# Optimization experiments

Hardware: AMD Instinct MI355X
Metric: run time of the kernel (lower is better)

## Reference

```python
import jax, jax.numpy as jnp
import numpy as np

N, M, ND, K = 80000, 150000, 10000, 27  # active voxels, 2D painted points, downscaled voxels, 3x3x3 kernel
C3, C2, CP = 16, 64, 259                # 3D ch (stage 1), 2D conv ch, painted 2D feature ch
CM, CO = C3 + C2, 32 + 64               # mixed ch (80), downscale out ch (96)


def subm_conv(feats, nbr, W):
    """Submanifold sparse conv as gather + per-offset GEMM.
    feats: [N_in, Cin], nbr: [N_out, K] int (-1 = missing), W: [K, Cin, Cout]."""
    out = jnp.zeros((nbr.shape[0], W.shape[-1]), feats.dtype)
    for k in range(W.shape[0]):  # fixed small kernel loop (27)
        idx = nbr[:, k]
        g = jnp.where((idx >= 0)[:, None], feats[jnp.clip(idx, 0)], 0.0)
        out = out + g @ W[k]
    return out


def bn_relu(x, gamma, beta):  # folded eval-mode BN1d + ReLU
    return jax.nn.relu(x * gamma + beta)


def setup_inputs() -> dict:
    key = jax.random.key(0)
    ks = jax.random.split(key, 24)

    def w(k, shape, fan_in):
        return jax.random.normal(k, shape, jnp.float32) * (1.0 / np.sqrt(fan_in))

    inp = {
        'x3d': jax.random.normal(ks[0], (N, C3), jnp.float32),
        'f2d': jax.random.normal(ks[1], (M, CP), jnp.float32),
        'nn_idx': jax.random.randint(ks[2], (N,), -1, M, jnp.int32),     # -1 = no 2D match
        'nbr': jax.random.randint(ks[3], (N, K), -1, N, jnp.int32),      # -1 = missing neighbor
        'nbr_ds': jax.random.randint(ks[4], (ND, K), -1, N, jnp.int32),
        'W3d': w(ks[5], (K, C3, C3), K * C3),
        'g3d': jnp.ones((C3,), jnp.float32), 'b3d': jnp.zeros((C3,), jnp.float32),
        'Wg': w(ks[6], (C3, CP), C3), 'bg': jnp.zeros((CP,), jnp.float32),
        'Wc': w(ks[7], (C3, CP), C3), 'bc': jnp.zeros((CP,), jnp.float32),
        'Wp': w(ks[8], (CP, C2), CP),
        'W2d': w(ks[9], (K, C2, C2), K * C2),
        'g2d': jnp.ones((C2,), jnp.float32), 'b2d': jnp.zeros((C2,), jnp.float32),
        'Wm1': w(ks[10], (K, CM, CM), K * CM),
        'gm1': jnp.ones((CM,), jnp.float32), 'bm1': jnp.zeros((CM,), jnp.float32),
        'Wm2': w(ks[11], (K, CM, CM), K * CM),
        'gm2': jnp.ones((CM,), jnp.float32), 'bm2': jnp.zeros((CM,), jnp.float32),
        'Wa1': w(ks[12], (K, CM, CM), K * CM),
        'ga1': jnp.ones((CM,), jnp.float32), 'ba1': jnp.zeros((CM,), jnp.float32),
        'Wa2': w(ks[13], (K, CM, CM), K * CM),
        'ga2': jnp.ones((CM,), jnp.float32), 'ba2': jnp.zeros((CM,), jnp.float32),
        'Wds': w(ks[14], (K, CM, CO), K * CM),
        'gds': jnp.ones((CO,), jnp.float32), 'bds': jnp.zeros((CO,), jnp.float32),
    }
    return inp


def reference(x3d, f2d, nn_idx, nbr, nbr_ds,
              W3d, g3d, b3d, Wg, bg, Wc, bc, Wp,
              W2d, g2d, b2d,
              Wm1, gm1, bm1, Wm2, gm2, bm2,
              Wa1, ga1, ba1, Wa2, ga2, ba2,
              Wds, gds, bds):
    # irregular gather of painted 2D features to voxel sites (NN index, -1 invalid)
    f2g = jnp.where((nn_idx >= 0)[:, None], f2d[jnp.clip(nn_idx, 0)], 0.0)  # [N, 259]

    # 3D branch: SubMConv3d(C3->C3) + BN + ReLU
    y3d = bn_relu(subm_conv(x3d, nbr, W3d), g3d, b3d)                       # [N, 16]

    # per-stage gate / cross-gate (Linear + ReLU) on 3D features, applied to raw 2D feats
    gate = jax.nn.relu(y3d @ Wg + bg)                                       # [N, 259]
    cross = jax.nn.relu(y3d @ Wc + bc)                                      # [N, 259]

    # gated 2D branch: project gated painted feats to 64, SubMConv3d + BN + ReLU
    p2d = (gate * f2g) @ Wp                                                 # [N, 64]
    x2d = bn_relu(subm_conv(p2d, nbr, W2d), g2d, b2d)                       # [N, 64]
    cross2d = (cross * f2g) @ Wp                                            # [N, 64]

    # cross-modal mix + SparseBasicBlock (residual, two subm convs)
    mix = jnp.concatenate([y3d, x2d + cross2d], axis=-1)                    # [N, 80]
    h = bn_relu(subm_conv(mix, nbr, Wm1), gm1, bm1)
    h = jax.nn.relu(subm_conv(h, nbr, Wm2) * gm2 + bm2 + mix)

    # aggregation SparseBasicBlock
    a = bn_relu(subm_conv(h, nbr, Wa1), ga1, ba1)
    a = jax.nn.relu(subm_conv(a, nbr, Wa2) * ga2 + ba2 + h)

    # strided SparseConv3d downscale (gather from input sites at new out sites)
    out = bn_relu(subm_conv(a, nbr_ds, Wds), gds, bds)                      # [ND, 96]
    return out
```

## Files before the change

kernel.cpp:

```cpp
#include <hip/hip_runtime.h>

#define NPTS 80000
#define MPTS 150000
#define NDPTS 10000
#define KOFF 27
#define C3 16
#define CP 259
#define C2 64
#define CM 80
#define CO 96

typedef __attribute__((ext_vector_type(8))) short short8;
typedef __attribute__((ext_vector_type(4))) float f32x4;

__device__ inline short bf16r(float f) {
  union { float f; unsigned u; } x{f};
  unsigned r = (x.u + 0x7fffu + ((x.u >> 16) & 1u)) >> 16;
  return (short)r;
}

__global__ void wfrag_kernel(const float* __restrict__ W, short* __restrict__ WbfF,
                             int CIN, int COUT_, int KC) {
  const int NT = COUT_ / 16;
  int i = blockIdx.x * 256 + threadIdx.x;
  int total = KOFF * KC * NT * 512;
  if (i >= total) return;
  int j = i & 7, lane = (i >> 3) & 63;
  int rest = i >> 9;
  int t = rest % NT; rest /= NT;
  int q = rest % KC;
  int k = rest / KC;
  int ci = q * 32 + (lane >> 4) * 8 + j;
  int n = t * 16 + (lane & 15);
  float v = (ci < CIN) ? W[((size_t)k * CIN + ci) * COUT_ + n] : 0.f;
  WbfF[i] = bf16r(v);
}

__global__ void wpfrag_kernel(const float* __restrict__ Wp, short* __restrict__ WpF) {
  int i = blockIdx.x * 256 + threadIdx.x;
  if (i >= 9 * 4 * 64 * 8) return;
  int j = i & 7, lane = (i >> 3) & 63, t = (i >> 9) & 3, q = i >> 11;
  int k = q * 32 + (lane >> 4) * 8 + j;
  int n = t * 16 + (lane & 15);
  WpF[i] = (k < CP) ? bf16r(Wp[(size_t)k * C2 + n]) : (short)0;
}

__global__ __launch_bounds__(256) void conv3d_bnrelu_kernel(
    const float* __restrict__ x3d, const int* __restrict__ nbr,
    const float* __restrict__ W3d, const float* __restrict__ g3d,
    const float* __restrict__ b3d, float* __restrict__ y3d,
    float* __restrict__ mix, short* __restrict__ mixbf)
{
  __shared__ float wS[KOFF * C3 * C3];
  __shared__ float fS[16][C3];
  const int tid = threadIdx.x;
  const int base = blockIdx.x * 16;
  for (int e = tid; e < KOFF * C3 * C3; e += 256) wS[e] = W3d[e];
  const int r = tid >> 4, c = tid & 15;
  const int row = base + r;
  float acc = 0.f;
  for (int k = 0; k < KOFF; ++k) {
    int idx = nbr[row * KOFF + k];
    float fv = (idx >= 0) ? x3d[idx * C3 + c] : 0.f;
    __syncthreads();
    fS[r][c] = fv;
    __syncthreads();
    const float* wk = &wS[k * C3 * C3];
    #pragma unroll
    for (int ci = 0; ci < C3; ++ci)
      acc = fmaf(fS[r][ci], wk[ci * C3 + c], acc);
  }
  float v = fmaxf(fmaf(acc, g3d[c], b3d[c]), 0.f);
  y3d[row * C3 + c] = v;
  mix[row * CM + c] = v;
  mixbf[row * CM + c] = bf16r(v);
}

__global__ __launch_bounds__(256) void gate_cross_mfma_kernel(
    const float* __restrict__ y3d, const float* __restrict__ f2d,
    const int* __restrict__ nn_idx,
    const float* __restrict__ Wg, const float* __restrict__ bg,
    const float* __restrict__ Wc, const float* __restrict__ bc,
    const short* __restrict__ WpF,
    short* __restrict__ p2dbf, float* __restrict__ cross2d)
{
  constexpr int RS = 296;
  __shared__ short g1S[32 * RS];
  __shared__ short g2S[32 * RS];
  const int tid = threadIdx.x;
  const int lane = tid & 63;
  const int w = tid >> 6;
  const int lm = lane & 15;
  const int quad = lane >> 4;
  const int base = blockIdx.x * 32;

  for (int e = tid; e < 32 * 32; e += 256) {
    int r = e >> 5, cc = 256 + (e & 31);
    if (cc >= CP) {
      g1S[r * RS + cc] = 0;
      g2S[r * RS + cc] = 0;
    }
  }

  {
    const int c = tid;
    float wg[16], wc[16];
    #pragma unroll
    for (int ci = 0; ci < 16; ++ci) {
      wg[ci] = Wg[ci * CP + c];
      wc[ci] = Wc[ci * CP + c];
    }
    const float bgv = bg[c], bcv = bc[c];
    for (int r = 0; r < 32; ++r) {
      const int row = base + r;
      const int idx = nn_idx[row];
      const float* yr = y3d + (size_t)row * C3;
      float f = (idx >= 0) ? f2d[(size_t)idx * CP + c] : 0.f;
      float a1 = bgv, a2 = bcv;
      #pragma unroll
      for (int ci = 0; ci < 16; ++ci) {
        float yv = yr[ci];
        a1 = fmaf(yv, wg[ci], a1);
        a2 = fmaf(yv, wc[ci], a2);
      }
      g1S[r * RS + c] = bf16r(fmaxf(a1, 0.f) * f);
      g2S[r * RS + c] = bf16r(fmaxf(a2, 0.f) * f);
    }
  }
  if (w == 0 && lane < 3) {
    const int c = 256 + lane;
    float wg[16], wc[16];
    #pragma unroll
    for (int ci = 0; ci < 16; ++ci) {
      wg[ci] = Wg[ci * CP + c];
      wc[ci] = Wc[ci * CP + c];
    }
    const float bgv = bg[c], bcv = bc[c];
    for (int r = 0; r < 32; ++r) {
      const int row = base + r;
      const int idx = nn_idx[row];
      const float* yr = y3d + (size_t)row * C3;
      float f = (idx >= 0) ? f2d[(size_t)idx * CP + c] : 0.f;
      float a1 = bgv, a2 = bcv;
      #pragma unroll
      for (int ci = 0; ci < 16; ++ci) {
        float yv = yr[ci];
        a1 = fmaf(yv, wg[ci], a1);
        a2 = fmaf(yv, wc[ci], a2);
      }
      g1S[r * RS + c] = bf16r(fmaxf(a1, 0.f) * f);
      g2S[r * RS + c] = bf16r(fmaxf(a2, 0.f) * f);
    }
  }
  __syncthreads();

  const int gsel = w & 1;
  const int mt = w >> 1;
  const short* gS = gsel ? g2S : g1S;
  f32x4 acc[4];
  #pragma unroll
  for (int t = 0; t < 4; ++t) {
    f32x4 z = {0.f, 0.f, 0.f, 0.f};
    acc[t] = z;
  }
  #pragma unroll
  for (int q = 0; q < 9; ++q) {
    short8 af = *(const short8*)&gS[(mt * 16 + lm) * RS + q * 32 + quad * 8];
    #pragma unroll
    for (int t = 0; t < 4; ++t) {
      short8 bf = *(const short8*)&WpF[(((q * 4 + t) * 64) + lane) * 8];
      acc[t] = __builtin_amdgcn_mfma_f32_16x16x32_bf16(af, bf, acc[t], 0, 0, 0);
    }
  }
  #pragma unroll
  for (int t = 0; t < 4; ++t) {
    const int c = t * 16 + lm;
    #pragma unroll
    for (int rg = 0; rg < 4; ++rg) {
      const int row = base + mt * 16 + quad * 4 + rg;
      float v = acc[t][rg];
      if (gsel == 0)
        p2dbf[(size_t)row * C2 + c] = bf16r(v);
      else
        cross2d[(size_t)row * C2 + c] = v;
    }
  }
}

template <int CIN, int COUT_, int MODE, int MINW>
__global__ __launch_bounds__(256, MINW) void conv_db_kernel(
    const short* __restrict__ finbf, const int* __restrict__ nbr, int nrows,
    const short* __restrict__ WbfF, const float* __restrict__ gamma,
    const float* __restrict__ beta, const float* __restrict__ resf,
    float* __restrict__ outf, short* __restrict__ outbf)
{
  constexpr int KC = (CIN + 31) / 32;
  constexpr int KC32 = KC * 32;
  constexpr int AS = KC32 + 8;
  constexpr int PCH = KC32 / 8;
  constexpr int DCH = CIN / 8;
  constexpr int NT = COUT_ / 16;
  constexpr int MT = 2;
  constexpr int ROWS = 128;
  constexpr int AR = ROWS * PCH / 256;

  __shared__ short fA[2][ROWS * AS];

  const int tid = threadIdx.x;
  const int lane = tid & 63;
  const int w = tid >> 6;
  const int lm = lane & 15;
  const int quad = lane >> 4;
  const int base = blockIdx.x * ROWS;

  int ar[AR], ac[AR];
  #pragma unroll
  for (int i = 0; i < AR; ++i) {
    int j = tid + i * 256;
    ar[i] = j / PCH;
    ac[i] = j - ar[i] * PCH;
  }

  f32x4 acc[MT][NT];
  #pragma unroll
  for (int i = 0; i < MT; ++i)
    #pragma unroll
    for (int t = 0; t < NT; ++t) {
      f32x4 z = {0.f, 0.f, 0.f, 0.f};
      acc[i][t] = z;
    }

  const short8 zero8 = {0, 0, 0, 0, 0, 0, 0, 0};
  short8 pa[AR];

  #pragma unroll
  for (int i = 0; i < AR; ++i) {
    int row = base + ar[i];
    int ix = (row < nrows) ? nbr[(size_t)row * KOFF] : -1;
    pa[i] = (ix >= 0 && ac[i] < DCH)
        ? *(const short8*)&finbf[(size_t)ix * CIN + ac[i] * 8] : zero8;
  }
  #pragma unroll
  for (int i = 0; i < AR; ++i)
    *(short8*)&fA[0][ar[i] * AS + ac[i] * 8] = pa[i];
  __syncthreads();

  for (int k = 0; k < KOFF; ++k) {
    const int cur = k & 1;
    if (k + 1 < KOFF) {
      #pragma unroll
      for (int i = 0; i < AR; ++i) {
        int row = base + ar[i];
        int ix = (row < nrows) ? nbr[(size_t)row * KOFF + k + 1] : -1;
        pa[i] = (ix >= 0 && ac[i] < DCH)
            ? *(const short8*)&finbf[(size_t)ix * CIN + ac[i] * 8] : zero8;
      }
    }
    #pragma unroll
    for (int q = 0; q < KC; ++q) {
      short8 afr[MT];
      #pragma unroll
      for (int i = 0; i < MT; ++i)
        afr[i] = *(const short8*)&fA[cur][((w * MT + i) * 16 + lm) * AS +
                                          q * 32 + quad * 8];
      #pragma unroll
      for (int t = 0; t < NT; ++t) {
        short8 bfr = *(const short8*)&WbfF[(size_t)(((k * KC + q) * NT + t) * 512) +
                                           lane * 8];
        #pragma unroll
        for (int i = 0; i < MT; ++i)
          acc[i][t] = __builtin_amdgcn_mfma_f32_16x16x32_bf16(afr[i], bfr,
                                                              acc[i][t], 0, 0, 0);
      }
    }
    if (k + 1 < KOFF) {
      #pragma unroll
      for (int i = 0; i < AR; ++i)
        *(short8*)&fA[cur ^ 1][ar[i] * AS + ac[i] * 8] = pa[i];
    }
    __syncthreads();
  }

  #pragma unroll
  for (int i = 0; i < MT; ++i) {
    int rbase = base + (w * MT + i) * 16 + quad * 4;
    #pragma unroll
    for (int t = 0; t < NT; ++t) {
      int c = t * 16 + lm;
      float g = gamma[c], b = beta[c];
      #pragma unroll
      for (int rg = 0; rg < 4; ++rg) {
        int row = rbase + rg;
        if (row >= nrows) continue;
        float v = acc[i][t][rg];
        if (MODE == 0) {
          outf[(size_t)row * COUT_ + c] = fmaxf(fmaf(v, g, b), 0.f);
        } else if (MODE == 1) {
          outbf[(size_t)row * COUT_ + c] = bf16r(fmaxf(fmaf(v, g, b), 0.f));
        } else if (MODE == 2) {
          float o = fmaxf(fmaf(v, g, b), 0.f) + resf[(size_t)row * C2 + c];
          outf[(size_t)row * CM + 16 + c] = o;
          outbf[(size_t)row * CM + 16 + c] = bf16r(o);
        } else if (MODE == 3) {
          float o = fmaxf(fmaf(v, g, b) + resf[(size_t)row * COUT_ + c], 0.f);
          outf[(size_t)row * COUT_ + c] = o;
          outbf[(size_t)row * COUT_ + c] = bf16r(o);
        } else {
          float o = fmaxf(fmaf(v, g, b) + resf[(size_t)row * COUT_ + c], 0.f);
          outbf[(size_t)row * COUT_ + c] = bf16r(o);
        }
      }
    }
  }
}

extern "C" void kernel_launch(void* const* d_in, const int* in_sizes, int n_in,
                              void* d_out, int out_size, void* d_ws, size_t ws_size,
                              hipStream_t stream) {
  const float* x3d  = (const float*)d_in[0];
  const float* f2d  = (const float*)d_in[1];
  const int*   nn   = (const int*)d_in[2];
  const int*   nbr  = (const int*)d_in[3];
  const int*   nbds = (const int*)d_in[4];
  const float* W3d  = (const float*)d_in[5];
  const float* g3d  = (const float*)d_in[6];
  const float* b3d  = (const float*)d_in[7];
  const float* Wg   = (const float*)d_in[8];
  const float* bg   = (const float*)d_in[9];
  const float* Wc   = (const float*)d_in[10];
  const float* bc   = (const float*)d_in[11];
  const float* Wp   = (const float*)d_in[12];
  const float* W2d  = (const float*)d_in[13];
  const float* g2d  = (const float*)d_in[14];
  const float* b2d  = (const float*)d_in[15];
  const float* Wm1  = (const float*)d_in[16];
  const float* gm1  = (const float*)d_in[17];
  const float* bm1  = (const float*)d_in[18];
  const float* Wm2  = (const float*)d_in[19];
  const float* gm2  = (const float*)d_in[20];
  const float* bm2  = (const float*)d_in[21];
  const float* Wa1  = (const float*)d_in[22];
  const float* ga1  = (const float*)d_in[23];
  const float* ba1  = (const float*)d_in[24];
  const float* Wa2  = (const float*)d_in[25];
  const float* ga2  = (const float*)d_in[26];
  const float* ba2  = (const float*)d_in[27];
  const float* Wds  = (const float*)d_in[28];
  const float* gds  = (const float*)d_in[29];
  const float* bds  = (const float*)d_in[30];

  const size_t N = NPTS;
  float* ws = (float*)d_ws;
  float* y3d     = ws;
  short* p2dbf   = (short*)(ws + N * 16);
  float* cross2d = ws + N * 48;
  float* mix     = ws + N * 112;
  short* mixbf   = (short*)(ws + N * 192);
  short* tmp1bf  = (short*)(ws + N * 232);
  float* hbuf    = ws + N * 272;
  short* hbufbf  = (short*)(ws + N * 352);
  short* abufbf  = (short*)ws;
  short* wtail  = (short*)(ws + N * 392);
  short* WbfF2d = wtail;
  short* WbfFm1 = WbfF2d + 110592;
  short* WbfFm2 = WbfFm1 + 207360;
  short* WbfFa1 = WbfFm2 + 207360;
  short* WbfFa2 = WbfFa1 + 207360;
  short* WbfFds = WbfFa2 + 207360;
  short* WpF    = WbfFds + 248832;

  wfrag_kernel<<<(110592 + 255) / 256, 256, 0, stream>>>(W2d, WbfF2d, 64, 64, 2);
  wfrag_kernel<<<(207360 + 255) / 256, 256, 0, stream>>>(Wm1, WbfFm1, 80, 80, 3);
  wfrag_kernel<<<(207360 + 255) / 256, 256, 0, stream>>>(Wm2, WbfFm2, 80, 80, 3);
  wfrag_kernel<<<(207360 + 255) / 256, 256, 0, stream>>>(Wa1, WbfFa1, 80, 80, 3);
  wfrag_kernel<<<(207360 + 255) / 256, 256, 0, stream>>>(Wa2, WbfFa2, 80, 80, 3);
  wfrag_kernel<<<(248832 + 255) / 256, 256, 0, stream>>>(Wds, WbfFds, 80, 96, 3);
  wpfrag_kernel<<<(9 * 4 * 64 * 8 + 255) / 256, 256, 0, stream>>>(Wp, WpF);

  conv3d_bnrelu_kernel<<<NPTS / 16, 256, 0, stream>>>(x3d, nbr, W3d, g3d, b3d,
                                                      y3d, mix, mixbf);
  gate_cross_mfma_kernel<<<NPTS / 32, 256, 0, stream>>>(y3d, f2d, nn, Wg, bg,
                                                        Wc, bc, WpF, p2dbf,
                                                        cross2d);

  const int gridN = (NPTS + 127) / 128;
  conv_db_kernel<64, 64, 2, 4><<<gridN, 256, 0, stream>>>(
      p2dbf, nbr, NPTS, WbfF2d, g2d, b2d, cross2d, mix, mixbf);
  conv_db_kernel<80, 80, 1, 3><<<gridN, 256, 0, stream>>>(
      mixbf, nbr, NPTS, WbfFm1, gm1, bm1, nullptr, nullptr, tmp1bf);
  conv_db_kernel<80, 80, 3, 3><<<gridN, 256, 0, stream>>>(
      tmp1bf, nbr, NPTS, WbfFm2, gm2, bm2, mix, hbuf, hbufbf);
  conv_db_kernel<80, 80, 1, 3><<<gridN, 256, 0, stream>>>(
      hbufbf, nbr, NPTS, WbfFa1, ga1, ba1, nullptr, nullptr, tmp1bf);
  conv_db_kernel<80, 80, 4, 3><<<gridN, 256, 0, stream>>>(
      tmp1bf, nbr, NPTS, WbfFa2, ga2, ba2, hbuf, nullptr, abufbf);

  const int gridND = (NDPTS + 127) / 128;
  conv_db_kernel<80, 96, 0, 3><<<gridND, 256, 0, stream>>>(
      abufbf, nbds, NDPTS, WbfFds, gds, bds, nullptr, (float*)d_out, nullptr);
}
```

Measured before the change: 1.136 ms.

## Replace LDS double-buffered sparse conv with register-direct gather and triple-buffered prefetch

The sparse conv kernel no longer stages gathered neighbor rows through shared memory. Each 64-thread wave loads its MFMA A-fragments straight from global memory into registers, using a three-stage rotation of register buffers and neighbor indices to prefetch offsets ahead of the MFMAs. This removes the LDS writes and reads and the per-offset __syncthreads. In exchange it raises register pressure, and the gathers are narrower and less coalesced. Blocks shrink to one wave covering 32 rows, which gives many more small blocks.

```diff
diff --git a/kernel.cpp b/kernel.cpp
--- a/kernel.cpp
+++ b/kernel.cpp
@@ -187,38 +187,29 @@
   }
 }
 
-template <int CIN, int COUT_, int MODE, int MINW>
-__global__ __launch_bounds__(256, MINW) void conv_db_kernel(
+template <int CIN, int COUT_, int MODE>
+__global__ __launch_bounds__(64, 2) void conv_nolds_kernel(
     const short* __restrict__ finbf, const int* __restrict__ nbr, int nrows,
     const short* __restrict__ WbfF, const float* __restrict__ gamma,
     const float* __restrict__ beta, const float* __restrict__ resf,
     float* __restrict__ outf, short* __restrict__ outbf)
 {
   constexpr int KC = (CIN + 31) / 32;
-  constexpr int KC32 = KC * 32;
-  constexpr int AS = KC32 + 8;
-  constexpr int PCH = KC32 / 8;
   constexpr int DCH = CIN / 8;
   constexpr int NT = COUT_ / 16;
   constexpr int MT = 2;
-  constexpr int ROWS = 128;
-  constexpr int AR = ROWS * PCH / 256;
-
-  __shared__ short fA[2][ROWS * AS];
-
-  const int tid = threadIdx.x;
-  const int lane = tid & 63;
-  const int w = tid >> 6;
+
+  const int lane = threadIdx.x;
   const int lm = lane & 15;
   const int quad = lane >> 4;
-  const int base = blockIdx.x * ROWS;
-
-  int ar[AR], ac[AR];
-  #pragma unroll
-  for (int i = 0; i < AR; ++i) {
-    int j = tid + i * 256;
-    ar[i] = j / PCH;
-    ac[i] = j - ar[i] * PCH;
+  const int base = blockIdx.x * (MT * 16);
+
+  int rrow[MT];
+  bool rok[MT];
+  #pragma unroll
+  for (int i = 0; i < MT; ++i) {
+    rrow[i] = base + i * 16 + lm;
+    rok[i] = rrow[i] < nrows;
   }
 
   f32x4 acc[MT][NT];
@@ -231,59 +222,63 @@
     }
 
   const short8 zero8 = {0, 0, 0, 0, 0, 0, 0, 0};
-  short8 pa[AR];
-
-  #pragma unroll
-  for (int i = 0; i < AR; ++i) {
-    int row = base + ar[i];
-    int ix = (row < nrows) ? nbr[(size_t)row * KOFF] : -1;
-    pa[i] = (ix >= 0 && ac[i] < DCH)
-        ? *(const short8*)&finbf[(size_t)ix * CIN + ac[i] * 8] : zero8;
-  }
-  #pragma unroll
-  for (int i = 0; i < AR; ++i)
-    *(short8*)&fA[0][ar[i] * AS + ac[i] * 8] = pa[i];
-  __syncthreads();
-
-  for (int k = 0; k < KOFF; ++k) {
-    const int cur = k & 1;
-    if (k + 1 < KOFF) {
-      #pragma unroll
-      for (int i = 0; i < AR; ++i) {
-        int row = base + ar[i];
-        int ix = (row < nrows) ? nbr[(size_t)row * KOFF + k + 1] : -1;
-        pa[i] = (ix >= 0 && ac[i] < DCH)
-            ? *(const short8*)&finbf[(size_t)ix * CIN + ac[i] * 8] : zero8;
-      }
-    }
+
+  auto loadIdx = [&](int (&id)[MT], int k) {
+    #pragma unroll
+    for (int i = 0; i < MT; ++i)
+      id[i] = (k < KOFF && rok[i]) ? nbr[(size_t)rrow[i] * KOFF + k] : -1;
+  };
+
+  auto loadA = [&](short8 (&pa)[MT][KC], const int (&id)[MT]) {
+    #pragma unroll
+    for (int i = 0; i < MT; ++i) {
+      const int safe = (id[i] < 0) ? 0 : id[i];
+      const bool ok = id[i] >= 0;
+      const short* src = finbf + (size_t)safe * CIN;
+      #pragma unroll
+      for (int q = 0; q < KC; ++q) {
+        const int ch = q * 4 + quad;
+        short8 v = zero8;
+        if (ch < DCH) v = *(const short8*)(src + ch * 8);
+        pa[i][q] = ok ? v : zero8;
+      }
+    }
+  };
+
+  auto computeK = [&](const short8 (&pa)[MT][KC], int k) {
+    const short* wb = WbfF + ((size_t)k * KC * NT) * 512 + lane * 8;
     #pragma unroll
     for (int q = 0; q < KC; ++q) {
-      short8 afr[MT];
-      #pragma unroll
-      for (int i = 0; i < MT; ++i)
-        afr[i] = *(const short8*)&fA[cur][((w * MT + i) * 16 + lm) * AS +
-                                          q * 32 + quad * 8];
       #pragma unroll
       for (int t = 0; t < NT; ++t) {
-        short8 bfr = *(const short8*)&WbfF[(size_t)(((k * KC + q) * NT + t) * 512) +
-                                           lane * 8];
+        short8 bfr = *(const short8*)(wb + (q * NT + t) * 512);
         #pragma unroll
         for (int i = 0; i < MT; ++i)
-          acc[i][t] = __builtin_amdgcn_mfma_f32_16x16x32_bf16(afr[i], bfr,
+          acc[i][t] = __builtin_amdgcn_mfma_f32_16x16x32_bf16(pa[i][q], bfr,
                                                               acc[i][t], 0, 0, 0);
       }
     }
-    if (k + 1 < KOFF) {
-      #pragma unroll
-      for (int i = 0; i < AR; ++i)
-        *(short8*)&fA[cur ^ 1][ar[i] * AS + ac[i] * 8] = pa[i];
-    }
-    __syncthreads();
+  };
+
+  int ia[MT], ib[MT], ic[MT];
+  short8 paA[MT][KC], paB[MT][KC], paC[MT][KC];
+
+  loadIdx(ia, 0); loadIdx(ib, 1); loadIdx(ic, 2);
+  loadA(paA, ia); loadIdx(ia, 3);
+  loadA(paB, ib); loadIdx(ib, 4);
+
+  for (int kk = 0; kk < KOFF; kk += 3) {
+    loadA(paC, ic); loadIdx(ic, kk + 5);
+    computeK(paA, kk);
+    loadA(paA, ia); loadIdx(ia, kk + 6);
+    computeK(paB, kk + 1);
+    loadA(paB, ib); loadIdx(ib, kk + 7);
+    computeK(paC, kk + 2);
   }
 
   #pragma unroll
   for (int i = 0; i < MT; ++i) {
-    int rbase = base + (w * MT + i) * 16 + quad * 4;
+    int rbase = base + i * 16 + quad * 4;
     #pragma unroll
     for (int t = 0; t < NT; ++t) {
       int c = t * 16 + lm;
@@ -383,19 +378,19 @@
                                                         Wc, bc, WpF, p2dbf,
                                                         cross2d);
 
-  const int gridN = (NPTS + 127) / 128;
-  conv_db_kernel<64, 64, 2, 4><<<gridN, 256, 0, stream>>>(
+  const int gridW = (NPTS + 31) / 32;
+  conv_nolds_kernel<64, 64, 2><<<gridW, 64, 0, stream>>>(
       p2dbf, nbr, NPTS, WbfF2d, g2d, b2d, cross2d, mix, mixbf);
-  conv_db_kernel<80, 80, 1, 3><<<gridN, 256, 0, stream>>>(
+  conv_nolds_kernel<80, 80, 1><<<gridW, 64, 0, stream>>>(
       mixbf, nbr, NPTS, WbfFm1, gm1, bm1, nullptr, nullptr, tmp1bf);
-  conv_db_kernel<80, 80, 3, 3><<<gridN, 256, 0, stream>>>(
+  conv_nolds_kernel<80, 80, 3><<<gridW, 64, 0, stream>>>(
       tmp1bf, nbr, NPTS, WbfFm2, gm2, bm2, mix, hbuf, hbufbf);
-  conv_db_kernel<80, 80, 1, 3><<<gridN, 256, 0, stream>>>(
+  conv_nolds_kernel<80, 80, 1><<<gridW, 64, 0, stream>>>(
       hbufbf, nbr, NPTS, WbfFa1, ga1, ba1, nullptr, nullptr, tmp1bf);
-  conv_db_kernel<80, 80, 4, 3><<<gridN, 256, 0, stream>>>(
+  conv_nolds_kernel<80, 80, 4><<<gridW, 64, 0, stream>>>(
       tmp1bf, nbr, NPTS, WbfFa2, ga2, ba2, hbuf, nullptr, abufbf);
 
-  const int gridND = (NDPTS + 127) / 128;
-  conv_db_kernel<80, 96, 0, 3><<<gridND, 256, 0, stream>>>(
+  const int gridDS = (NDPTS + 31) / 32;
+  conv_nolds_kernel<80, 96, 0><<<gridDS, 64, 0, stream>>>(
       abufbf, nbds, NDPTS, WbfFds, gds, bds, nullptr, (float*)d_out, nullptr);
 }
```

Result: faster. 1.094 ms (-3.7%).
